# Performance work log

Hardware: AMD Instinct MI355X
Metric: run time of the kernel (lower is better)

## Reference

```python
import jax, jax.numpy as jnp
import numpy as np

N, E = 50000, 800000
F_IN, HID, NCLS = 128, 128, 64
EPS = 1e-6


def setup_inputs() -> dict:
    key = jax.random.key(0)
    ks = jax.random.split(key, 6)
    x = jax.random.normal(ks[0], (N, F_IN), dtype=jnp.float32)
    edge_index = jax.random.randint(ks[1], (2, E), 0, N, dtype=jnp.int32)
    # GCNConv glorot init
    W1 = jax.random.normal(ks[2], (F_IN, HID), dtype=jnp.float32) * np.sqrt(2.0 / (F_IN + HID))
    b1 = jnp.zeros((HID,), jnp.float32)
    gamma1 = jnp.ones((HID,), jnp.float32)
    beta1 = jnp.zeros((HID,), jnp.float32)
    W2 = jax.random.normal(ks[3], (HID, NCLS), dtype=jnp.float32) * np.sqrt(2.0 / (HID + NCLS))
    b2 = jnp.zeros((NCLS,), jnp.float32)
    return {"x": x, "edge_index": edge_index, "W1": W1, "b1": b1,
            "gamma1": gamma1, "beta1": beta1, "W2": W2, "b2": b2}


def _gcn_conv(x, src, dst, norm, W, b, n):
    # x' = A_hat @ (x W) + b, A_hat = D^-1/2 (A+I) D^-1/2
    h = x @ W                                   # [N, out]
    msg = h[src] * norm[:, None]                # [E+N, out] gather
    out = jax.ops.segment_sum(msg, dst, num_segments=n)  # scatter-add
    return out + b


def _layer_norm(h, gamma, beta):
    mu = jnp.mean(h, axis=-1, keepdims=True)
    var = jnp.mean(jnp.square(h - mu), axis=-1, keepdims=True)
    return (h - mu) * jax.lax.rsqrt(var + EPS) * gamma + beta


def reference(x, edge_index, W1, b1, gamma1, beta1, W2, b2):
    n = x.shape[0]
    loop = jnp.arange(n, dtype=edge_index.dtype)
    src = jnp.concatenate([edge_index[0], loop])  # add self loops
    dst = jnp.concatenate([edge_index[1], loop])
    deg = jax.ops.segment_sum(jnp.ones_like(dst, jnp.float32), dst, num_segments=n)
    dinv = jnp.where(deg > 0, jax.lax.rsqrt(deg), 0.0)
    norm = dinv[src] * dinv[dst]                 # [E+N]
    h = _gcn_conv(x, src, dst, norm, W1, b1, n)
    h = jax.nn.relu(_layer_norm(h, gamma1, beta1))
    out = _gcn_conv(h, src, dst, norm, W2, b2, n)
    return out
```

## Files before the change

### kernel.cpp

```cpp
#include <hip/hip_runtime.h>


typedef float f32x2 __attribute__((ext_vector_type(2)));
typedef float f32x4 __attribute__((ext_vector_type(4)));
typedef __bf16 bf16x8 __attribute__((ext_vector_type(8)));

__device__ __forceinline__ unsigned short f2bf(float f) {
    unsigned u = __float_as_uint(f);
    u += 0x7FFF + ((u >> 16) & 1);
    return (unsigned short)(u >> 16);
}
__device__ __forceinline__ float bfLo(unsigned g) { return __uint_as_float(g << 16); }
__device__ __forceinline__ float bfHi(unsigned g) { return __uint_as_float(g & 0xFFFF0000u); }

__global__ __launch_bounds__(256) void cvt_wi(const float* __restrict__ W1,
                                              const float* __restrict__ W2,
                                              unsigned short* __restrict__ W1t,
                                              unsigned short* __restrict__ W2t,
                                              int* __restrict__ cnt, int n) {
    int id = blockIdx.x * 256 + threadIdx.x;
    if (id < 128 * 128) {
        int c = id >> 7, k = id & 127;
        W1t[id] = f2bf(W1[k * 128 + c]);
    } else if (id < 128 * 128 + 64 * 128) {
        int j = id - 128 * 128;
        int c = j >> 7, k = j & 127;
        W2t[j] = f2bf(W2[k * 64 + c]);
    }
    if (id < n) cnt[id] = 0;
}

__global__ __launch_bounds__(256) void cvt_x(const float4* __restrict__ x4,
                                             uint4* __restrict__ xb4, int total) {
    int i = blockIdx.x * 256 + threadIdx.x;
    if (i >= total) return;
    float4 v0 = x4[2 * i], v1 = x4[2 * i + 1];
    uint4 o;
    o.x = (unsigned)f2bf(v0.x) | ((unsigned)f2bf(v0.y) << 16);
    o.y = (unsigned)f2bf(v0.z) | ((unsigned)f2bf(v0.w) << 16);
    o.z = (unsigned)f2bf(v1.x) | ((unsigned)f2bf(v1.y) << 16);
    o.w = (unsigned)f2bf(v1.z) | ((unsigned)f2bf(v1.w) << 16);
    xb4[i] = o;
}

__global__ void count_k(const int* __restrict__ dst, int* __restrict__ cnt,
                        int* __restrict__ rank, int e) {
    int i = blockIdx.x * blockDim.x + threadIdx.x;
    if (i < e) {
        int r = atomicAdd(&cnt[dst[i]], 1);
        __builtin_nontemporal_store(r, &rank[i]);
    }
}

__global__ __launch_bounds__(1024) void scan1_k(const int* __restrict__ cnt,
                                                int* __restrict__ incl,
                                                int* __restrict__ bsum, int n) {
    __shared__ int lds[1024];
    int t = threadIdx.x;
    int i = blockIdx.x * 1024 + t;
    int v = (i < n) ? cnt[i] : 0;
    lds[t] = v;
    __syncthreads();
#pragma unroll
    for (int d = 1; d < 1024; d <<= 1) {
        int u = (t >= d) ? lds[t - d] : 0;
        __syncthreads();
        lds[t] += u;
        __syncthreads();
    }
    if (i < n) incl[i] = lds[t];
    if (t == 1023) bsum[blockIdx.x] = lds[1023];
}

__global__ __launch_bounds__(64) void scan2_k(const int* __restrict__ bsum,
                                              int* __restrict__ bpre, int nb) {
    int t = threadIdx.x;
    int v = (t < nb) ? bsum[t] : 0;
#pragma unroll
    for (int d = 1; d < 64; d <<= 1) {
        int u = __shfl_up(v, d);
        if (t >= d) v += u;
    }
    if (t < nb) bpre[t] = v - bsum[t];
}

__global__ __launch_bounds__(1024) void scan3_k(const int* __restrict__ cnt,
                                                const int* __restrict__ incl,
                                                const int* __restrict__ bpre,
                                                int* __restrict__ offs,
                                                float* __restrict__ dinv, int n) {
    int i = blockIdx.x * 1024 + threadIdx.x;
    if (i >= n) return;
    int c = cnt[i];
    int inc = incl[i] + bpre[blockIdx.x];
    offs[i] = inc - c;
    dinv[i] = rsqrtf((float)(c + 1));
    if (i == n - 1) offs[n] = inc;
}

__global__ void fill_k(const int* __restrict__ src, const int* __restrict__ dst,
                       const int* __restrict__ rank, const int* __restrict__ offs,
                       const float* __restrict__ dinv,
                       unsigned* __restrict__ epk, int e) {
    int i = blockIdx.x * blockDim.x + threadIdx.x;
    if (i >= e) return;
    int s = src[i], d = dst[i];
    float w = dinv[s] * dinv[d];
    epk[offs[d] + rank[i]] = ((unsigned)s << 16) | (unsigned)f2bf(w);
}

template<int NT>
__global__ __launch_bounds__(256) void gemm_mfma(const uint4* __restrict__ Ab,
                                                 const uint4* __restrict__ Wt,
                                                 unsigned short* __restrict__ tab,
                                                 int n) {
    __shared__ uint4 As[64 * 16];
    int t = threadIdx.x;
    int r0 = blockIdx.x * 64;
    int rows = min(64, n - r0);
#pragma unroll
    for (int it = 0; it < 4; ++it) {
        int u = it * 256 + t;
        int row = u >> 4, s = u & 15;
        uint4 v = make_uint4(0u, 0u, 0u, 0u);
        if (row < rows) v = Ab[(size_t)(r0 + row) * 16 + s];
        As[row * 16 + (s ^ (row & 7))] = v;
    }
    __syncthreads();

    int wv = t >> 6, lane = t & 63;
    int arow = lane & 15;
    int kg = lane >> 4;
    int lrow = wv * 16 + arow;

    f32x4 acc[NT];
    f32x4 z = {0.f, 0.f, 0.f, 0.f};
#pragma unroll
    for (int j = 0; j < NT; ++j) acc[j] = z;

#pragma unroll
    for (int ks = 0; ks < 4; ++ks) {
        bf16x8 a = __builtin_bit_cast(bf16x8,
                       As[lrow * 16 + ((ks * 4 + kg) ^ (arow & 7))]);
#pragma unroll
        for (int tl = 0; tl < NT; ++tl) {
            bf16x8 b = __builtin_bit_cast(bf16x8,
                           Wt[(size_t)(tl * 16 + arow) * 16 + ks * 4 + kg]);
            acc[tl] = __builtin_amdgcn_mfma_f32_16x16x32_bf16(a, b, acc[tl], 0, 0, 0);
        }
    }

    int grow0 = r0 + wv * 16 + 4 * kg;
#pragma unroll
    for (int r = 0; r < 4; ++r) {
        int grow = grow0 + r;
        if (grow < n) {
            unsigned short* rowp = tab + (size_t)grow * (NT * 16) + arow;
#pragma unroll
            for (int tl = 0; tl < NT; ++tl)
                rowp[tl * 16] = f2bf(acc[tl][r]);
        }
    }
}

__global__ __launch_bounds__(256) void prop_ln(const unsigned* __restrict__ h0b,
                                               const int* __restrict__ offs,
                                               const unsigned* __restrict__ epk,
                                               const float* __restrict__ dinv,
                                               const float* __restrict__ b1,
                                               const float* __restrict__ gamma,
                                               const float* __restrict__ beta,
                                               unsigned* __restrict__ h1b, int n) {
    int wid = __builtin_amdgcn_readfirstlane((blockIdx.x * blockDim.x + threadIdx.x) >> 6);
    int lane = threadIdx.x & 63;
    if (wid >= n) return;
    float di = dinv[wid];
    unsigned self = h0b[(size_t)wid * 64 + lane];
    float a0 = bfLo(self) * di * di;
    float a1 = bfHi(self) * di * di;

    int s0 = offs[wid], s1 = offs[wid + 1];
    if (s0 < s1) {
        int k = s0;
        int sj[8]; float wj[8];
#pragma unroll
        for (int j = 0; j < 8; ++j) {
            int idx = k + j;
            unsigned p = __builtin_nontemporal_load(&epk[min(idx, s1 - 1)]);
            sj[j] = (int)(p >> 16);
            wj[j] = (idx < s1) ? bfLo(p) : 0.f;
        }
        while (k < s1) {
            unsigned g[8];
#pragma unroll
            for (int j = 0; j < 8; ++j) g[j] = h0b[(size_t)sj[j] * 64 + lane];
            k += 8;
            int s2[8]; float w2[8];
#pragma unroll
            for (int j = 0; j < 8; ++j) {
                int idx = k + j;
                unsigned p = __builtin_nontemporal_load(&epk[min(max(idx, s0), s1 - 1)]);
                s2[j] = (int)(p >> 16);
                w2[j] = (idx < s1) ? bfLo(p) : 0.f;
            }
#pragma unroll
            for (int j = 0; j < 8; ++j) {
                a0 = fmaf(bfLo(g[j]), wj[j], a0);
                a1 = fmaf(bfHi(g[j]), wj[j], a1);
            }
#pragma unroll
            for (int j = 0; j < 8; ++j) { sj[j] = s2[j]; wj[j] = w2[j]; }
        }
    }

    a0 += b1[2 * lane];
    a1 += b1[2 * lane + 1];
    float sum = a0 + a1, sq = a0 * a0 + a1 * a1;
#pragma unroll
    for (int off = 32; off > 0; off >>= 1) {
        sum += __shfl_xor(sum, off);
        sq  += __shfl_xor(sq, off);
    }
    float mu  = sum * (1.f / 128.f);
    float var = fmaxf(sq * (1.f / 128.f) - mu * mu, 0.f);
    float rstd = rsqrtf(var + 1e-6f);
    float y0 = fmaxf((a0 - mu) * rstd * gamma[2 * lane] + beta[2 * lane], 0.f);
    float y1 = fmaxf((a1 - mu) * rstd * gamma[2 * lane + 1] + beta[2 * lane + 1], 0.f);
    unsigned pk = (unsigned)f2bf(y0) | ((unsigned)f2bf(y1) << 16);
    __builtin_nontemporal_store(pk, &h1b[(size_t)wid * 64 + lane]);
}

__global__ __launch_bounds__(256) void prop_out(const unsigned* __restrict__ h2b,
                                                const int* __restrict__ offs,
                                                const unsigned* __restrict__ epk,
                                                const float* __restrict__ dinv,
                                                const float* __restrict__ b2,
                                                float* __restrict__ out, int n) {
    int wid = __builtin_amdgcn_readfirstlane((blockIdx.x * blockDim.x + threadIdx.x) >> 6);
    int lane = threadIdx.x & 63;
    if (wid >= n) return;
    int es = lane >> 5, u = lane & 31;
    float di = dinv[wid];
    float a0 = 0.f, a1 = 0.f;
    if (es == 0) {
        unsigned self = h2b[(size_t)wid * 32 + u];
        a0 = bfLo(self) * di * di;
        a1 = bfHi(self) * di * di;
    }

    int s0 = offs[wid], s1 = offs[wid + 1];
    if (s0 < s1) {
        int k = s0;
        int sj[8]; float wj[8];
#pragma unroll
        for (int j = 0; j < 8; ++j) {
            int idx = k + 2 * j + es;
            unsigned p = __builtin_nontemporal_load(&epk[min(idx, s1 - 1)]);
            sj[j] = (int)(p >> 16);
            wj[j] = (idx < s1) ? bfLo(p) : 0.f;
        }
        while (k < s1) {
            unsigned g[8];
#pragma unroll
            for (int j = 0; j < 8; ++j) g[j] = h2b[(size_t)sj[j] * 32 + u];
            k += 16;
            int s2[8]; float w2[8];
#pragma unroll
            for (int j = 0; j < 8; ++j) {
                int idx = k + 2 * j + es;
                unsigned p = __builtin_nontemporal_load(&epk[min(max(idx, s0), s1 - 1)]);
                s2[j] = (int)(p >> 16);
                w2[j] = (idx < s1) ? bfLo(p) : 0.f;
            }
#pragma unroll
            for (int j = 0; j < 8; ++j) {
                a0 = fmaf(bfLo(g[j]), wj[j], a0);
                a1 = fmaf(bfHi(g[j]), wj[j], a1);
            }
#pragma unroll
            for (int j = 0; j < 8; ++j) { sj[j] = s2[j]; wj[j] = w2[j]; }
        }
    }

    a0 += __shfl_xor(a0, 32);
    a1 += __shfl_xor(a1, 32);
    if (es == 0) {
        f32x2 o; o.x = a0 + b2[2 * u]; o.y = a1 + b2[2 * u + 1];
        __builtin_nontemporal_store(o, &((f32x2*)out)[(size_t)wid * 32 + u]);
    }
}

extern "C" void kernel_launch(void* const* d_in, const int* in_sizes, int n_in,
                              void* d_out, int out_size, void* d_ws, size_t ws_size,
                              hipStream_t stream) {
    const float* x     = (const float*)d_in[0];
    const int*   ei    = (const int*)d_in[1];
    const float* W1    = (const float*)d_in[2];
    const float* b1    = (const float*)d_in[3];
    const float* gam   = (const float*)d_in[4];
    const float* bet   = (const float*)d_in[5];
    const float* W2    = (const float*)d_in[6];
    const float* b2    = (const float*)d_in[7];
    float* out = (float*)d_out;

    int n = in_sizes[0] / 128;
    int e = in_sizes[1] / 2;
    const int* src = ei;
    const int* dst = ei + e;

    char* p = (char*)d_ws;
    auto alloc = [&](size_t bytes) {
        void* q = (void*)p;
        p += (bytes + 255) & ~(size_t)255;
        return q;
    };
    int*            cnt   = (int*)alloc((size_t)n * 4);
    int*            offs  = (int*)alloc((size_t)(n + 1) * 4);
    int*            rank  = (int*)alloc((size_t)e * 4);
    float*          dinv  = (float*)alloc((size_t)n * 4);
    unsigned*       epk   = (unsigned*)alloc((size_t)e * 4);
    unsigned*       h0b   = (unsigned*)alloc((size_t)n * 64 * 4);
    char*           h1buf = (char*)alloc((size_t)n * 128 * 4);
    unsigned short* W1t   = (unsigned short*)alloc(128 * 128 * 2);
    unsigned short* W2t   = (unsigned short*)alloc(64 * 128 * 2);

    unsigned* h1b = (unsigned*)h1buf;
    uint4*    xb  = (uint4*)(h1buf + (size_t)n * 64 * 4);
    unsigned* h2b = h0b;
    int* incl = (int*)h0b;
    int* bsum = incl + n;
    int* bpre = bsum + 64;

    int nb = (n + 1023) / 1024;

    cvt_wi<<<(n + 255) / 256, 256, 0, stream>>>(W1, W2, W1t, W2t, cnt, n);
    cvt_x<<<(n * 16 + 255) / 256, 256, 0, stream>>>((const float4*)x, xb, n * 16);
    count_k<<<(e + 255) / 256, 256, 0, stream>>>(dst, cnt, rank, e);
    scan1_k<<<nb, 1024, 0, stream>>>(cnt, incl, bsum, n);
    scan2_k<<<1, 64, 0, stream>>>(bsum, bpre, nb);
    scan3_k<<<nb, 1024, 0, stream>>>(cnt, incl, bpre, offs, dinv, n);
    fill_k<<<(e + 255) / 256, 256, 0, stream>>>(src, dst, rank, offs, dinv, epk, e);

    int gb = (n + 63) / 64;
    gemm_mfma<8><<<gb, 256, 0, stream>>>(xb, (const uint4*)W1t,
                                         (unsigned short*)h0b, n);
    prop_ln<<<(n + 3) / 4, 256, 0, stream>>>(h0b, offs, epk, dinv, b1, gam, bet, h1b, n);
    gemm_mfma<4><<<gb, 256, 0, stream>>>((const uint4*)h1b, (const uint4*)W2t,
                                         (unsigned short*)h2b, n);
    prop_out<<<(n + 3) / 4, 256, 0, stream>>>(h2b, offs, epk, dinv, b2, out, n);
}
```

Before: 183.9 us.

## Pad CSR rows to multiples of eight and load edge descriptors as vectors

Each node's edge segment in the packed CSR array is rounded up to a multiple of 8 entries, zero-filled through a memset, so both propagation kernels can fetch descriptors as two 16-byte vector loads per batch with no bounds clamping or masking. This drops the per-edge min/max index math and the eight scalar loads per batch, and it keeps the software prefetch of the next batch. The cost is up to 7 padding edges per node (gathers of row 0 with weight 0), a larger edge buffer and an extra memset over it on every call.

```diff
diff --git a/kernel.cpp b/kernel.cpp
--- a/kernel.cpp
+++ b/kernel.cpp
@@ -3,6 +3,7 @@
 
 typedef float f32x2 __attribute__((ext_vector_type(2)));
 typedef float f32x4 __attribute__((ext_vector_type(4)));
+typedef unsigned u32x4 __attribute__((ext_vector_type(4)));
 typedef __bf16 bf16x8 __attribute__((ext_vector_type(8)));
 
 __device__ __forceinline__ unsigned short f2bf(float f) {
@@ -58,7 +59,7 @@
     __shared__ int lds[1024];
     int t = threadIdx.x;
     int i = blockIdx.x * 1024 + t;
-    int v = (i < n) ? cnt[i] : 0;
+    int v = (i < n) ? ((cnt[i] + 7) & ~7) : 0;
     lds[t] = v;
     __syncthreads();
 #pragma unroll
@@ -92,8 +93,9 @@
     int i = blockIdx.x * 1024 + threadIdx.x;
     if (i >= n) return;
     int c = cnt[i];
+    int c8 = (c + 7) & ~7;
     int inc = incl[i] + bpre[blockIdx.x];
-    offs[i] = inc - c;
+    offs[i] = inc - c8;
     dinv[i] = rsqrtf((float)(c + 1));
     if (i == n - 1) offs[n] = inc;
 }
@@ -181,35 +183,25 @@
 
     int s0 = offs[wid], s1 = offs[wid + 1];
     if (s0 < s1) {
-        int k = s0;
-        int sj[8]; float wj[8];
-#pragma unroll
-        for (int j = 0; j < 8; ++j) {
-            int idx = k + j;
-            unsigned p = __builtin_nontemporal_load(&epk[min(idx, s1 - 1)]);
-            sj[j] = (int)(p >> 16);
-            wj[j] = (idx < s1) ? bfLo(p) : 0.f;
-        }
-        while (k < s1) {
+        const u32x4* ep4 = (const u32x4*)(epk + s0);
+        int nb8 = (s1 - s0) >> 3;
+        u32x4 d0 = __builtin_nontemporal_load(ep4);
+        u32x4 d1 = __builtin_nontemporal_load(ep4 + 1);
+        for (int b = 0; b < nb8; ++b) {
+            unsigned dsc[8] = {d0.x, d0.y, d0.z, d0.w, d1.x, d1.y, d1.z, d1.w};
             unsigned g[8];
 #pragma unroll
-            for (int j = 0; j < 8; ++j) g[j] = h0b[(size_t)sj[j] * 64 + lane];
-            k += 8;
-            int s2[8]; float w2[8];
+            for (int j = 0; j < 8; ++j)
+                g[j] = h0b[(size_t)(dsc[j] >> 16) * 64 + lane];
+            int bn = (b + 1 < nb8) ? b + 1 : 0;
+            d0 = __builtin_nontemporal_load(ep4 + 2 * bn);
+            d1 = __builtin_nontemporal_load(ep4 + 2 * bn + 1);
 #pragma unroll
             for (int j = 0; j < 8; ++j) {
-                int idx = k + j;
-                unsigned p = __builtin_nontemporal_load(&epk[min(max(idx, s0), s1 - 1)]);
-                s2[j] = (int)(p >> 16);
-                w2[j] = (idx < s1) ? bfLo(p) : 0.f;
+                float w = bfLo(dsc[j]);
+                a0 = fmaf(bfLo(g[j]), w, a0);
+                a1 = fmaf(bfHi(g[j]), w, a1);
             }
-#pragma unroll
-            for (int j = 0; j < 8; ++j) {
-                a0 = fmaf(bfLo(g[j]), wj[j], a0);
-                a1 = fmaf(bfHi(g[j]), wj[j], a1);
-            }
-#pragma unroll
-            for (int j = 0; j < 8; ++j) { sj[j] = s2[j]; wj[j] = w2[j]; }
         }
     }
 
@@ -250,35 +242,27 @@
 
     int s0 = offs[wid], s1 = offs[wid + 1];
     if (s0 < s1) {
-        int k = s0;
-        int sj[8]; float wj[8];
-#pragma unroll
-        for (int j = 0; j < 8; ++j) {
-            int idx = k + 2 * j + es;
-            unsigned p = __builtin_nontemporal_load(&epk[min(idx, s1 - 1)]);
-            sj[j] = (int)(p >> 16);
-            wj[j] = (idx < s1) ? bfLo(p) : 0.f;
-        }
-        while (k < s1) {
-            unsigned g[8];
-#pragma unroll
-            for (int j = 0; j < 8; ++j) g[j] = h2b[(size_t)sj[j] * 32 + u];
-            k += 16;
-            int s2[8]; float w2[8];
-#pragma unroll
-            for (int j = 0; j < 8; ++j) {
-                int idx = k + 2 * j + es;
-                unsigned p = __builtin_nontemporal_load(&epk[min(max(idx, s0), s1 - 1)]);
-                s2[j] = (int)(p >> 16);
-                w2[j] = (idx < s1) ? bfLo(p) : 0.f;
+        const u32x4* ep4 = (const u32x4*)(epk + s0);
+        int nb8 = (s1 - s0) >> 3;
+        u32x4 d0 = __builtin_nontemporal_load(ep4);
+        u32x4 d1 = __builtin_nontemporal_load(ep4 + 1);
+        for (int b = 0; b < nb8; ++b) {
+            unsigned dsc[8] = {d0.x, d0.y, d0.z, d0.w, d1.x, d1.y, d1.z, d1.w};
+            unsigned dd[4], g[4];
+#pragma unroll
+            for (int j = 0; j < 4; ++j) {
+                dd[j] = es ? dsc[2 * j + 1] : dsc[2 * j];
+                g[j] = h2b[(size_t)(dd[j] >> 16) * 32 + u];
             }
-#pragma unroll
-            for (int j = 0; j < 8; ++j) {
-                a0 = fmaf(bfLo(g[j]), wj[j], a0);
-                a1 = fmaf(bfHi(g[j]), wj[j], a1);
+            int bn = (b + 1 < nb8) ? b + 1 : 0;
+            d0 = __builtin_nontemporal_load(ep4 + 2 * bn);
+            d1 = __builtin_nontemporal_load(ep4 + 2 * bn + 1);
+#pragma unroll
+            for (int j = 0; j < 4; ++j) {
+                float w = bfLo(dd[j]);
+                a0 = fmaf(bfLo(g[j]), w, a0);
+                a1 = fmaf(bfHi(g[j]), w, a1);
             }
-#pragma unroll
-            for (int j = 0; j < 8; ++j) { sj[j] = s2[j]; wj[j] = w2[j]; }
         }
     }
 
@@ -307,6 +291,7 @@
     int e = in_sizes[1] / 2;
     const int* src = ei;
     const int* dst = ei + e;
+    size_t ecap = (size_t)e + 8 * (size_t)n;
 
     char* p = (char*)d_ws;
     auto alloc = [&](size_t bytes) {
@@ -318,7 +303,7 @@
     int*            offs  = (int*)alloc((size_t)(n + 1) * 4);
     int*            rank  = (int*)alloc((size_t)e * 4);
     float*          dinv  = (float*)alloc((size_t)n * 4);
-    unsigned*       epk   = (unsigned*)alloc((size_t)e * 4);
+    unsigned*       epk   = (unsigned*)alloc(ecap * 4);
     unsigned*       h0b   = (unsigned*)alloc((size_t)n * 64 * 4);
     char*           h1buf = (char*)alloc((size_t)n * 128 * 4);
     unsigned short* W1t   = (unsigned short*)alloc(128 * 128 * 2);
@@ -333,6 +318,7 @@
 
     int nb = (n + 1023) / 1024;
 
+    (void)hipMemsetAsync(epk, 0, ecap * 4, stream);
     cvt_wi<<<(n + 255) / 256, 256, 0, stream>>>(W1, W2, W1t, W2t, cnt, n);
     cvt_x<<<(n * 16 + 255) / 256, 256, 0, stream>>>((const float4*)x, xb, n * 16);
     count_k<<<(e + 255) / 256, 256, 0, stream>>>(dst, cnt, rank, e);
```

After: 192.3 us. 1.05x slower.
